# Kernel optimization log

Hardware: AMD Instinct MI355X
Metric: run time of the kernel (lower is better)

The kernel has to match this reference:

```python
import jax, jax.numpy as jnp
import numpy as np

N, D, C, E, K = 100000, 64, 40, 1600000, 2

def setup_inputs() -> dict:
    key = jax.random.key(0)
    k1, k2, k3 = jax.random.split(key, 3)
    x = jax.random.normal(k1, (N, D), dtype=jnp.float32)
    edge_index = jax.random.randint(k2, (2, E), 0, N, dtype=jnp.int64)
    W = jax.random.normal(k3, (D, C), dtype=jnp.float32) * 0.05
    b = jnp.zeros((C,), dtype=jnp.float32)
    return {"x": x, "edge_index": edge_index, "W": W, "b": b}

def reference(x, edge_index, W, b):
    n = x.shape[0]
    self_loop = jnp.arange(n, dtype=edge_index.dtype)
    row = jnp.concatenate([edge_index[0], self_loop])  # [E+N]
    col = jnp.concatenate([edge_index[1], self_loop])  # [E+N]
    # degree over row (out-degree incl. self loops), as in torch_geometric.utils.degree
    deg = jax.ops.segment_sum(jnp.ones_like(row, dtype=x.dtype), row, num_segments=n)
    deg_inv_sqrt = jnp.where(deg > 0, jax.lax.rsqrt(deg), 0.0)
    norm = deg_inv_sqrt[row] * deg_inv_sqrt[col]  # [E+N]
    # K hops of SpMM: out[r] += norm_e * x[c] for each edge e=(r,c)
    for _ in range(K):
        x = jax.ops.segment_sum(norm[:, None] * x[col], row, num_segments=n)
    logits = x @ W + b  # [N, C]
    return jax.nn.log_softmax(logits, axis=1)
```

## Files before the change

### kernel.cpp

```cpp
#include <hip/hip_runtime.h>
#include <math.h>


#define D_FEAT 64
#define NCLS 40
#define BROWS 512
#define BROWS_LOG 9
#define BINCAP 10240
#define CSRCAP 12288
#define EPT 25

typedef float v2f __attribute__((ext_vector_type(2)));

__device__ __forceinline__ unsigned pack_bf16_2(float lo, float hi) {
    unsigned ulo = __float_as_uint(lo);
    unsigned uhi = __float_as_uint(hi);
    ulo = (ulo + 0x7fffu + ((ulo >> 16) & 1u)) >> 16;
    uhi = (uhi + 0x7fffu + ((uhi >> 16) & 1u)) & 0xffff0000u;
    return uhi | ulo;
}

__device__ __forceinline__ void acc2p(unsigned u, v2f& a) {
    v2f v;
    v.x = __uint_as_float(u << 16);
    v.y = __uint_as_float(u & 0xffff0000u);
    a += v;
}

__global__ __launch_bounds__(256) void bin_edges_kernel(const int* __restrict__ rows,
                                                        const int* __restrict__ cols,
                                                        int* __restrict__ bucket_cursor,
                                                        unsigned* __restrict__ bins,
                                                        int e, int nb) {
    __shared__ int cnt[512];
    for (int i = threadIdx.x; i < nb; i += 256) cnt[i] = 0;
    __syncthreads();
    int base = blockIdx.x * (256 * EPT) + threadIdx.x;
    int rr[EPT], cc[EPT];
#pragma unroll
    for (int k = 0; k < EPT; k++) {
        int idx = base + k * 256;
        if (idx < e) { rr[k] = rows[idx]; cc[k] = cols[idx]; }
        else { rr[k] = -1; cc[k] = 0; }
    }
#pragma unroll
    for (int k = 0; k < EPT; k++)
        if (rr[k] >= 0) atomicAdd(&cnt[rr[k] >> BROWS_LOG], 1);
    __syncthreads();
    for (int i = threadIdx.x; i < nb; i += 256) {
        int c = cnt[i];
        cnt[i] = (c > 0) ? atomicAdd(&bucket_cursor[i], c) : 0;
    }
    __syncthreads();
#pragma unroll
    for (int k = 0; k < EPT; k++) {
        if (rr[k] >= 0) {
            int b = rr[k] >> BROWS_LOG;
            int pos = atomicAdd(&cnt[b], 1);
            bins[(size_t)b * BINCAP + pos] =
                ((unsigned)(rr[k] & (BROWS - 1)) << 17) | (unsigned)cc[k];
        }
    }
}

__global__ __launch_bounds__(512) void build_csr_kernel(const unsigned* __restrict__ bins,
                                                        const int* __restrict__ bucket_cursor,
                                                        int* __restrict__ csr_col,
                                                        uint2* __restrict__ row_info,
                                                        float* __restrict__ dis,
                                                        int* __restrict__ perm, int n) {
    __shared__ int cnt[512];
    __shared__ int sm[512];
    __shared__ int cur[512];
    __shared__ int lcsr[CSRCAP];
    int b = blockIdx.x;
    int tid = threadIdx.x;
    int m = bucket_cursor[b];
    cnt[tid] = 0;
    __syncthreads();
    const unsigned* bp = bins + (size_t)b * BINCAP;
    for (int i = tid; i < m; i += 512) atomicAdd(&cnt[bp[i] >> 17], 1);
    __syncthreads();
    int c = cnt[tid];
    int padded = (c + 3) & ~3;
    int r = b * BROWS + tid;
    if (r < n) dis[r] = rsqrtf(1.0f + (float)c);
    sm[tid] = padded;
    __syncthreads();
    for (int off = 1; off < 512; off <<= 1) {
        int t = (tid >= off) ? sm[tid - off] : 0;
        __syncthreads();
        sm[tid] += t;
        __syncthreads();
    }
    int off0 = sm[tid] - padded;
    cur[tid] = off0;
    if (r < n) row_info[r] = make_uint2((unsigned)(b * CSRCAP + off0), (unsigned)padded);
    __syncthreads();
    for (int i = tid; i < m; i += 512) {
        unsigned u = bp[i];
        int pos = atomicAdd(&cur[u >> 17], 1);
        lcsr[pos] = (int)(u & 0x1FFFFu);
    }
    __syncthreads();
    if (r < n) {
        for (int j = c; j < padded; j++) lcsr[off0 + j] = n;
    }
    __syncthreads();
    int tot = sm[511];
    int4* cp4 = (int4*)(csr_col + (size_t)b * CSRCAP);
    const int4* l4 = (const int4*)lcsr;
    for (int i = tid; i < (tot >> 2); i += 512) cp4[i] = l4[i];

    __syncthreads();
    if (tid < 64) cnt[tid] = 0;
    __syncthreads();
    int bin = min(padded >> 2, 63);
    if (r < n) atomicAdd(&cnt[bin], 1);
    __syncthreads();
    if (tid < 64) sm[tid] = cnt[tid];
    __syncthreads();
    for (int off = 1; off < 64; off <<= 1) {
        int t = (tid >= off && tid < 64) ? sm[tid - off] : 0;
        __syncthreads();
        if (tid < 64) sm[tid] += t;
        __syncthreads();
    }
    if (tid < 64) cur[tid] = sm[tid] - cnt[tid];
    __syncthreads();
    if (r < n) {
        int rank = atomicAdd(&cur[bin], 1);
        perm[b * BROWS + rank] = r;
    } else {
        perm[b * BROWS + tid] = -1;
    }
}

__global__ __launch_bounds__(256) void sort_rows_kernel(int* __restrict__ csr_col,
                                                        const uint2* __restrict__ row_info,
                                                        int n) {
    int wid = (int)((blockIdx.x * blockDim.x + threadIdx.x) >> 6);
    int lane = threadIdx.x & 63;
    int r0 = wid * 2, r1 = r0 + 1;
    if (r0 >= n) return;
    uint2 i0 = row_info[r0];
    uint2 i1 = (r1 < n) ? row_info[r1] : make_uint2(0u, 0u);
    int p0 = (int)i0.y, p1 = (int)i1.y;
    if (p0 <= 32 && p1 <= 32) {
        int half = lane >> 5, hl = lane & 31;
        int base = half ? (int)i1.x : (int)i0.x;
        int pad  = half ? p1 : p0;
        int key = (hl < pad) ? csr_col[base + hl] : 0x7fffffff;
#pragma unroll
        for (int k = 2; k <= 32; k <<= 1) {
#pragma unroll
            for (int j = k >> 1; j > 0; j >>= 1) {
                int other = __shfl_xor(key, j, 64);
                bool takeMin = (((hl & j) == 0) == ((hl & k) == 0));
                int mn = min(key, other), mx = max(key, other);
                key = takeMin ? mn : mx;
            }
        }
        if (hl < pad) csr_col[base + hl] = key;
    } else {
        for (int t = 0; t < 2; t++) {
            int base = t ? (int)i1.x : (int)i0.x;
            int pad  = t ? p1 : p0;
            if (pad == 0) continue;
            if (pad <= 64) {
                int key = (lane < pad) ? csr_col[base + lane] : 0x7fffffff;
#pragma unroll
                for (int k = 2; k <= 64; k <<= 1) {
#pragma unroll
                    for (int j = k >> 1; j > 0; j >>= 1) {
                        int other = __shfl_xor(key, j, 64);
                        bool takeMin = (((lane & j) == 0) == ((lane & k) == 0));
                        int mn = min(key, other), mx = max(key, other);
                        key = takeMin ? mn : mx;
                    }
                }
                if (lane < pad) csr_col[base + lane] = key;
            } else if (lane == 0) {
                for (int i2 = 1; i2 < pad; i2++) {
                    int kk = csr_col[base + i2];
                    int j2 = i2 - 1;
                    while (j2 >= 0 && csr_col[base + j2] > kk) {
                        csr_col[base + j2 + 1] = csr_col[base + j2]; j2--;
                    }
                    csr_col[base + j2 + 1] = kk;
                }
            }
        }
    }
}

__global__ void scale_x_kernel(const float* __restrict__ x, const float* __restrict__ dis,
                               unsigned* __restrict__ xs0, unsigned* __restrict__ xs1, int n) {
    int i = blockIdx.x * blockDim.x + threadIdx.x;
    int total = (n + 1) * (D_FEAT / 2);
    if (i >= total) return;
    int node = i >> 5;
    if (node < n) {
        float s = dis[node];
        float2 v = ((const float2*)x)[i];
        xs0[i] = pack_bf16_2(s * v.x, s * v.y);
    } else {
        xs0[i] = 0u;
        xs1[i] = 0u;
    }
}

#define GATHER16(cp, xs_in, ql, base, len)                                  \
    uint2 u0, u1, u2, u3, u4, u5, u6, u7;                                   \
    uint2 u8, u9, u10, u11, u12, u13, u14, u15;                             \
    bool g0 = base < len, g1 = base + 4 < len;                              \
    bool g2 = base + 8 < len, g3 = base + 12 < len;                         \
    if (g0) {                                                               \
        uint4 cv = cp[(base >> 2) + 0];                                     \
        u0 = xs_in[cv.x * 16 + ql]; u1 = xs_in[cv.y * 16 + ql];             \
        u2 = xs_in[cv.z * 16 + ql]; u3 = xs_in[cv.w * 16 + ql];             \
    }                                                                       \
    if (g1) {                                                               \
        uint4 cv = cp[(base >> 2) + 1];                                     \
        u4 = xs_in[cv.x * 16 + ql]; u5 = xs_in[cv.y * 16 + ql];             \
        u6 = xs_in[cv.z * 16 + ql]; u7 = xs_in[cv.w * 16 + ql];             \
    }                                                                       \
    if (g2) {                                                               \
        uint4 cv = cp[(base >> 2) + 2];                                     \
        u8 = xs_in[cv.x * 16 + ql]; u9 = xs_in[cv.y * 16 + ql];             \
        u10 = xs_in[cv.z * 16 + ql]; u11 = xs_in[cv.w * 16 + ql];           \
    }                                                                       \
    if (g3) {                                                               \
        uint4 cv = cp[(base >> 2) + 3];                                     \
        u12 = xs_in[cv.x * 16 + ql]; u13 = xs_in[cv.y * 16 + ql];           \
        u14 = xs_in[cv.z * 16 + ql]; u15 = xs_in[cv.w * 16 + ql];           \
    }                                                                       \
    if (g0) {                                                               \
        acc2p(u0.x, hA01); acc2p(u0.y, hA23);                               \
        acc2p(u1.x, hA01); acc2p(u1.y, hA23);                               \
        acc2p(u2.x, hA01); acc2p(u2.y, hA23);                               \
        acc2p(u3.x, hA01); acc2p(u3.y, hA23);                               \
    }                                                                       \
    if (g1) {                                                               \
        acc2p(u4.x, hB01); acc2p(u4.y, hB23);                               \
        acc2p(u5.x, hB01); acc2p(u5.y, hB23);                               \
        acc2p(u6.x, hB01); acc2p(u6.y, hB23);                               \
        acc2p(u7.x, hB01); acc2p(u7.y, hB23);                               \
    }                                                                       \
    if (g2) {                                                               \
        acc2p(u8.x, hA01); acc2p(u8.y, hA23);                               \
        acc2p(u9.x, hA01); acc2p(u9.y, hA23);                               \
        acc2p(u10.x, hA01); acc2p(u10.y, hA23);                             \
        acc2p(u11.x, hA01); acc2p(u11.y, hA23);                             \
    }                                                                       \
    if (g3) {                                                               \
        acc2p(u12.x, hB01); acc2p(u12.y, hB23);                             \
        acc2p(u13.x, hB01); acc2p(u13.y, hB23);                             \
        acc2p(u14.x, hB01); acc2p(u14.y, hB23);                             \
        acc2p(u15.x, hB01); acc2p(u15.y, hB23);                             \
    }

__global__ __launch_bounds__(256, 6) void spmm_hop1_kernel(const uint2* __restrict__ xs_in,
                                                           uint2* __restrict__ xs_out,
                                                           const int* __restrict__ perm,
                                                           const uint2* __restrict__ row_info,
                                                           const int* __restrict__ csr_col,
                                                           const float* __restrict__ dis,
                                                           int n, int nperm) {
    int wave = (blockIdx.x * blockDim.x + threadIdx.x) >> 6;
    int lane = threadIdx.x & 63;
    int q = lane >> 4, ql = lane & 15;
    int pidx = wave * 4 + q;
    int r = (pidx < nperm) ? perm[pidx] : -1;
    bool valid = (r >= 0);
    int s = 0, len = 0;
    if (valid) { uint2 info = row_info[r]; s = (int)info.x; len = (int)info.y; }
    int maxlen = len;
    maxlen = max(maxlen, __shfl_xor(maxlen, 16, 64));
    maxlen = max(maxlen, __shfl_xor(maxlen, 32, 64));

    v2f hA01 = {0.f, 0.f}, hA23 = {0.f, 0.f};
    v2f hB01 = {0.f, 0.f}, hB23 = {0.f, 0.f};
    const uint4* cp = (const uint4*)(csr_col + s);
    for (int base = 0; base < maxlen; base += 16) {
        GATHER16(cp, xs_in, ql, base, len)
    }
    if (valid) {
        v2f h01 = hA01 + hB01;
        v2f h23 = hA23 + hB23;
        uint2 us = xs_in[r * 16 + ql];
        acc2p(us.x, h01); acc2p(us.y, h23);
        float dr = dis[r];
        float dr2 = dr * dr;
        xs_out[r * 16 + ql] = make_uint2(pack_bf16_2(dr2 * h01.x, dr2 * h01.y),
                                         pack_bf16_2(dr2 * h23.x, dr2 * h23.y));
    }
}

__global__ __launch_bounds__(256, 6) void spmm_logits_kernel(const uint2* __restrict__ xs_in,
                                                             const int* __restrict__ perm,
                                                             const uint2* __restrict__ row_info,
                                                             const int* __restrict__ csr_col,
                                                             const float* __restrict__ dis,
                                                             const float* __restrict__ W,
                                                             const float* __restrict__ b,
                                                             float* __restrict__ out,
                                                             int n, int nperm) {
    __shared__ float Wt[NCLS][D_FEAT + 4];
    __shared__ float bl[NCLS];
    __shared__ float hl[16][D_FEAT + 4];
    for (int i = threadIdx.x; i < D_FEAT * NCLS; i += 256) {
        int d = i / NCLS, cc = i - d * NCLS;
        Wt[cc][d] = W[i];
    }
    for (int i = threadIdx.x; i < NCLS; i += 256) bl[i] = b[i];
    __syncthreads();

    int wave = (blockIdx.x * blockDim.x + threadIdx.x) >> 6;
    int lane = threadIdx.x & 63;
    int q = lane >> 4, ql = lane & 15;
    int pidx = wave * 4 + q;
    int r = (pidx < nperm) ? perm[pidx] : -1;
    bool valid = (r >= 0);
    int s = 0, len = 0;
    if (valid) { uint2 info = row_info[r]; s = (int)info.x; len = (int)info.y; }
    int maxlen = len;
    maxlen = max(maxlen, __shfl_xor(maxlen, 16, 64));
    maxlen = max(maxlen, __shfl_xor(maxlen, 32, 64));

    v2f hA01 = {0.f, 0.f}, hA23 = {0.f, 0.f};
    v2f hB01 = {0.f, 0.f}, hB23 = {0.f, 0.f};
    const uint4* cp = (const uint4*)(csr_col + s);
    for (int base = 0; base < maxlen; base += 16) {
        GATHER16(cp, xs_in, ql, base, len)
    }

    float y0, y1, y2;
    int c0 = ql, c1 = ql + 16;
    int c2 = (ql < 8) ? (ql + 32) : ql;
    {
        v2f h01 = hA01 + hB01;
        v2f h23 = hA23 + hB23;
        uint2 us = valid ? xs_in[r * 16 + ql] : make_uint2(0u, 0u);
        acc2p(us.x, h01); acc2p(us.y, h23);
        float dr = valid ? dis[r] : 0.f;
        float h0 = h01.x * dr, h1 = h01.y * dr, h2 = h23.x * dr, h3 = h23.y * dr;

        int rowslot = ((threadIdx.x >> 6) << 2) + q;
        *(float4*)&hl[rowslot][ql * 4] = make_float4(h0, h1, h2, h3);

        y0 = bl[c0]; y1 = bl[c1]; y2 = bl[c2];
#pragma unroll
        for (int g = 0; g < 16; g++) {
            float4 hv = *(const float4*)&hl[rowslot][g * 4];
            float4 w0 = *(const float4*)&Wt[c0][g * 4];
            float4 w1 = *(const float4*)&Wt[c1][g * 4];
            float4 w2 = *(const float4*)&Wt[c2][g * 4];
            y0 += hv.x * w0.x + hv.y * w0.y + hv.z * w0.z + hv.w * w0.w;
            y1 += hv.x * w1.x + hv.y * w1.y + hv.z * w1.z + hv.w * w1.w;
            y2 += hv.x * w2.x + hv.y * w2.y + hv.z * w2.z + hv.w * w2.w;
        }
    }

    bool has3 = (ql < 8);
    float m = fmaxf(y0, y1);
    if (has3) m = fmaxf(m, y2);
#pragma unroll
    for (int o = 8; o > 0; o >>= 1) m = fmaxf(m, __shfl_xor(m, o, 64));
    float sm = __expf(y0 - m) + __expf(y1 - m) + (has3 ? __expf(y2 - m) : 0.f);
#pragma unroll
    for (int o = 8; o > 0; o >>= 1) sm += __shfl_xor(sm, o, 64);
    float lse = m + __logf(sm);

    if (valid) {
        float* op = out + (long long)r * NCLS;
        op[ql] = y0 - lse;
        op[ql + 16] = y1 - lse;
        if (has3) op[ql + 32] = y2 - lse;
    }
}

extern "C" void kernel_launch(void* const* d_in, const int* in_sizes, int n_in,
                              void* d_out, int out_size, void* d_ws, size_t ws_size,
                              hipStream_t stream) {
    const float* x  = (const float*)d_in[0];
    const int*   ei = (const int*)d_in[1];
    const float* W  = (const float*)d_in[2];
    const float* b  = (const float*)d_in[3];
    float* out = (float*)d_out;

    const int n = in_sizes[0] / D_FEAT;
    const int e = in_sizes[1] / 2;
    const int nb = (n + BROWS - 1) / BROWS;

    const int* rows = ei;
    const int* cols = ei + e;

    size_t na = ((size_t)n + 256) & ~(size_t)255;
    size_t npm = (size_t)nb * BROWS;
    int*      bucket_cursor = (int*)d_ws;
    float*    dis           = (float*)(bucket_cursor + 256);
    uint2*    row_info      = (uint2*)(dis + na);
    int*      perm          = (int*)(row_info + na);
    unsigned* bins          = (unsigned*)(perm + npm);
    int*      csr_col       = (int*)(bins + (size_t)nb * BINCAP);
    unsigned* xs0           = (unsigned*)(csr_col + (size_t)nb * CSRCAP);
    unsigned* xs1           = xs0 + (size_t)(n + 1) * (D_FEAT / 2);

    const int BS = 256;

    hipMemsetAsync(bucket_cursor, 0, (size_t)nb * sizeof(int), stream);
    {
        int blocks = (e + BS * EPT - 1) / (BS * EPT);
        bin_edges_kernel<<<blocks, BS, 0, stream>>>(rows, cols, bucket_cursor, bins, e, nb);
    }
    build_csr_kernel<<<nb, 512, 0, stream>>>(bins, bucket_cursor, csr_col, row_info, dis,
                                             perm, n);
    {
        int nwv = (n + 1) / 2;
        int blocks = (nwv * 64 + BS - 1) / BS;
        sort_rows_kernel<<<blocks, BS, 0, stream>>>(csr_col, row_info, n);
    }
    {
        int tot = (n + 1) * (D_FEAT / 2);
        scale_x_kernel<<<(tot + BS - 1) / BS, BS, 0, stream>>>(x, dis, xs0, xs1, n);
    }

    int nperm = (int)npm;
    int nwaves = nperm / 4;
    int blocks = (nwaves * 64 + BS - 1) / BS;
    spmm_hop1_kernel<<<blocks, BS, 0, stream>>>((const uint2*)xs0, (uint2*)xs1, perm,
                                                row_info, csr_col, dis, n, nperm);
    spmm_logits_kernel<<<blocks, BS, 0, stream>>>((const uint2*)xs1, perm, row_info, csr_col,
                                                  dis, W, b, out, n, nperm);
}
```

Before: 211.0 us.

## Pack per-row info, merge sort and scale kernels, prefetch column indices

Replaces the perm array plus the row_info and dis lookups with a packed uint4 per permuted slot (offset, length, row, degree scale), removing a dependent indirection at the start of each SpMM wave. The sort and x-scaling kernels are merged into one launch, split by block index. The gather loop now software-prefetches the next 16 column indices while gathering the current ones. Gathers are issued without per-group guards, relying on padding of the CSR tail with the dummy node. Occupancy hint drops from 6 to 5 to make room for the extra prefetch registers.

```diff
diff --git a/kernel.cpp b/kernel.cpp
--- a/kernel.cpp
+++ b/kernel.cpp
@@ -68,7 +68,7 @@
                                                         int* __restrict__ csr_col,
                                                         uint2* __restrict__ row_info,
                                                         float* __restrict__ dis,
-                                                        int* __restrict__ perm, int n) {
+                                                        uint4* __restrict__ pinfo, int n) {
     __shared__ int cnt[512];
     __shared__ int sm[512];
     __shared__ int cur[512];
@@ -84,7 +84,8 @@
     int c = cnt[tid];
     int padded = (c + 3) & ~3;
     int r = b * BROWS + tid;
-    if (r < n) dis[r] = rsqrtf(1.0f + (float)c);
+    float dv = rsqrtf(1.0f + (float)c);
+    if (r < n) dis[r] = dv;
     sm[tid] = padded;
     __syncthreads();
     for (int off = 1; off < 512; off <<= 1) {
@@ -111,6 +112,10 @@
     int4* cp4 = (int4*)(csr_col + (size_t)b * CSRCAP);
     const int4* l4 = (const int4*)lcsr;
     for (int i = tid; i < (tot >> 2); i += 512) cp4[i] = l4[i];
+    {
+        int g = tot + tid;
+        if (g < CSRCAP) csr_col[(size_t)b * CSRCAP + g] = n;
+    }
 
     __syncthreads();
     if (tid < 64) cnt[tid] = 0;
@@ -130,16 +135,37 @@
     __syncthreads();
     if (r < n) {
         int rank = atomicAdd(&cur[bin], 1);
-        perm[b * BROWS + rank] = r;
+        pinfo[b * BROWS + rank] = make_uint4((unsigned)(b * CSRCAP + off0),
+                                             (unsigned)padded, (unsigned)r,
+                                             __float_as_uint(dv));
     } else {
-        perm[b * BROWS + tid] = -1;
-    }
-}
-
-__global__ __launch_bounds__(256) void sort_rows_kernel(int* __restrict__ csr_col,
-                                                        const uint2* __restrict__ row_info,
-                                                        int n) {
-    int wid = (int)((blockIdx.x * blockDim.x + threadIdx.x) >> 6);
+        pinfo[b * BROWS + tid] = make_uint4(0u, 0u, 0xFFFFFFFFu, 0u);
+    }
+}
+
+__global__ __launch_bounds__(256) void sort_scale_kernel(int* __restrict__ csr_col,
+                                                         const uint2* __restrict__ row_info,
+                                                         const float* __restrict__ x,
+                                                         const float* __restrict__ dis,
+                                                         unsigned* __restrict__ xs0,
+                                                         unsigned* __restrict__ xs1,
+                                                         int n, int sortBlocks) {
+    if ((int)blockIdx.x >= sortBlocks) {
+        int i = ((int)blockIdx.x - sortBlocks) * 256 + threadIdx.x;
+        int total = (n + 1) * (D_FEAT / 2);
+        if (i >= total) return;
+        int node = i >> 5;
+        if (node < n) {
+            float s = dis[node];
+            float2 v = ((const float2*)x)[i];
+            xs0[i] = pack_bf16_2(s * v.x, s * v.y);
+        } else {
+            xs0[i] = 0u;
+            xs1[i] = 0u;
+        }
+        return;
+    }
+    int wid = ((int)blockIdx.x * 256 + (int)threadIdx.x) >> 6;
     int lane = threadIdx.x & 63;
     int r0 = wid * 2, r1 = r0 + 1;
     if (r0 >= n) return;
@@ -194,87 +220,59 @@
     }
 }
 
-__global__ void scale_x_kernel(const float* __restrict__ x, const float* __restrict__ dis,
-                               unsigned* __restrict__ xs0, unsigned* __restrict__ xs1, int n) {
-    int i = blockIdx.x * blockDim.x + threadIdx.x;
-    int total = (n + 1) * (D_FEAT / 2);
-    if (i >= total) return;
-    int node = i >> 5;
-    if (node < n) {
-        float s = dis[node];
-        float2 v = ((const float2*)x)[i];
-        xs0[i] = pack_bf16_2(s * v.x, s * v.y);
-    } else {
-        xs0[i] = 0u;
-        xs1[i] = 0u;
-    }
-}
-
-#define GATHER16(cp, xs_in, ql, base, len)                                  \
-    uint2 u0, u1, u2, u3, u4, u5, u6, u7;                                   \
-    uint2 u8, u9, u10, u11, u12, u13, u14, u15;                             \
-    bool g0 = base < len, g1 = base + 4 < len;                              \
-    bool g2 = base + 8 < len, g3 = base + 12 < len;                         \
-    if (g0) {                                                               \
-        uint4 cv = cp[(base >> 2) + 0];                                     \
-        u0 = xs_in[cv.x * 16 + ql]; u1 = xs_in[cv.y * 16 + ql];             \
-        u2 = xs_in[cv.z * 16 + ql]; u3 = xs_in[cv.w * 16 + ql];             \
+#define GATHER_ITER(cp, xs_in, ql, base, len)                               \
+    uint2 u0 = xs_in[cv0.x * 16 + ql], u1 = xs_in[cv0.y * 16 + ql];         \
+    uint2 u2 = xs_in[cv0.z * 16 + ql], u3 = xs_in[cv0.w * 16 + ql];         \
+    uint2 u4 = xs_in[cv1.x * 16 + ql], u5 = xs_in[cv1.y * 16 + ql];         \
+    uint2 u6 = xs_in[cv1.z * 16 + ql], u7 = xs_in[cv1.w * 16 + ql];         \
+    uint2 u8 = xs_in[cv2.x * 16 + ql], u9 = xs_in[cv2.y * 16 + ql];         \
+    uint2 u10 = xs_in[cv2.z * 16 + ql], u11 = xs_in[cv2.w * 16 + ql];       \
+    uint2 u12 = xs_in[cv3.x * 16 + ql], u13 = xs_in[cv3.y * 16 + ql];       \
+    uint2 u14 = xs_in[cv3.z * 16 + ql], u15 = xs_in[cv3.w * 16 + ql];       \
+    {                                                                       \
+        int nb4 = (base >> 2) + 4;                                          \
+        nv0 = cp[nb4]; nv1 = cp[nb4 + 1];                                   \
+        nv2 = cp[nb4 + 2]; nv3 = cp[nb4 + 3];                               \
     }                                                                       \
-    if (g1) {                                                               \
-        uint4 cv = cp[(base >> 2) + 1];                                     \
-        u4 = xs_in[cv.x * 16 + ql]; u5 = xs_in[cv.y * 16 + ql];             \
-        u6 = xs_in[cv.z * 16 + ql]; u7 = xs_in[cv.w * 16 + ql];             \
-    }                                                                       \
-    if (g2) {                                                               \
-        uint4 cv = cp[(base >> 2) + 2];                                     \
-        u8 = xs_in[cv.x * 16 + ql]; u9 = xs_in[cv.y * 16 + ql];             \
-        u10 = xs_in[cv.z * 16 + ql]; u11 = xs_in[cv.w * 16 + ql];           \
-    }                                                                       \
-    if (g3) {                                                               \
-        uint4 cv = cp[(base >> 2) + 3];                                     \
-        u12 = xs_in[cv.x * 16 + ql]; u13 = xs_in[cv.y * 16 + ql];           \
-        u14 = xs_in[cv.z * 16 + ql]; u15 = xs_in[cv.w * 16 + ql];           \
-    }                                                                       \
-    if (g0) {                                                               \
+    __builtin_amdgcn_sched_barrier(0);                                      \
+    if (base < len) {                                                       \
         acc2p(u0.x, hA01); acc2p(u0.y, hA23);                               \
         acc2p(u1.x, hA01); acc2p(u1.y, hA23);                               \
         acc2p(u2.x, hA01); acc2p(u2.y, hA23);                               \
         acc2p(u3.x, hA01); acc2p(u3.y, hA23);                               \
     }                                                                       \
-    if (g1) {                                                               \
+    if (base + 4 < len) {                                                   \
         acc2p(u4.x, hB01); acc2p(u4.y, hB23);                               \
         acc2p(u5.x, hB01); acc2p(u5.y, hB23);                               \
         acc2p(u6.x, hB01); acc2p(u6.y, hB23);                               \
         acc2p(u7.x, hB01); acc2p(u7.y, hB23);                               \
     }                                                                       \
-    if (g2) {                                                               \
+    if (base + 8 < len) {                                                   \
         acc2p(u8.x, hA01); acc2p(u8.y, hA23);                               \
         acc2p(u9.x, hA01); acc2p(u9.y, hA23);                               \
         acc2p(u10.x, hA01); acc2p(u10.y, hA23);                             \
         acc2p(u11.x, hA01); acc2p(u11.y, hA23);                             \
     }                                                                       \
-    if (g3) {                                                               \
+    if (base + 12 < len) {                                                  \
         acc2p(u12.x, hB01); acc2p(u12.y, hB23);                             \
         acc2p(u13.x, hB01); acc2p(u13.y, hB23);                             \
         acc2p(u14.x, hB01); acc2p(u14.y, hB23);                             \
         acc2p(u15.x, hB01); acc2p(u15.y, hB23);                             \
-    }
-
-__global__ __launch_bounds__(256, 6) void spmm_hop1_kernel(const uint2* __restrict__ xs_in,
+    }                                                                       \
+    cv0 = nv0; cv1 = nv1; cv2 = nv2; cv3 = nv3;
+
+__global__ __launch_bounds__(256, 5) void spmm_hop1_kernel(const uint2* __restrict__ xs_in,
                                                            uint2* __restrict__ xs_out,
-                                                           const int* __restrict__ perm,
-                                                           const uint2* __restrict__ row_info,
+                                                           const uint4* __restrict__ pinfo,
                                                            const int* __restrict__ csr_col,
-                                                           const float* __restrict__ dis,
-                                                           int n, int nperm) {
+                                                           int n) {
     int wave = (blockIdx.x * blockDim.x + threadIdx.x) >> 6;
     int lane = threadIdx.x & 63;
     int q = lane >> 4, ql = lane & 15;
-    int pidx = wave * 4 + q;
-    int r = (pidx < nperm) ? perm[pidx] : -1;
+    uint4 info = pinfo[wave * 4 + q];
+    int s = (int)info.x, len = (int)info.y;
+    int r = (int)info.z;
     bool valid = (r >= 0);
-    int s = 0, len = 0;
-    if (valid) { uint2 info = row_info[r]; s = (int)info.x; len = (int)info.y; }
     int maxlen = len;
     maxlen = max(maxlen, __shfl_xor(maxlen, 16, 64));
     maxlen = max(maxlen, __shfl_xor(maxlen, 32, 64));
@@ -282,30 +280,30 @@
     v2f hA01 = {0.f, 0.f}, hA23 = {0.f, 0.f};
     v2f hB01 = {0.f, 0.f}, hB23 = {0.f, 0.f};
     const uint4* cp = (const uint4*)(csr_col + s);
+    uint4 cv0 = cp[0], cv1 = cp[1], cv2 = cp[2], cv3 = cp[3];
+    uint4 nv0, nv1, nv2, nv3;
     for (int base = 0; base < maxlen; base += 16) {
-        GATHER16(cp, xs_in, ql, base, len)
+        GATHER_ITER(cp, xs_in, ql, base, len)
     }
     if (valid) {
         v2f h01 = hA01 + hB01;
         v2f h23 = hA23 + hB23;
         uint2 us = xs_in[r * 16 + ql];
         acc2p(us.x, h01); acc2p(us.y, h23);
-        float dr = dis[r];
-        float dr2 = dr * dr;
-        xs_out[r * 16 + ql] = make_uint2(pack_bf16_2(dr2 * h01.x, dr2 * h01.y),
-                                         pack_bf16_2(dr2 * h23.x, dr2 * h23.y));
-    }
-}
-
-__global__ __launch_bounds__(256, 6) void spmm_logits_kernel(const uint2* __restrict__ xs_in,
-                                                             const int* __restrict__ perm,
-                                                             const uint2* __restrict__ row_info,
+        float dr = __uint_as_float(info.w);
+        float d2 = dr * dr;
+        xs_out[r * 16 + ql] = make_uint2(pack_bf16_2(d2 * h01.x, d2 * h01.y),
+                                         pack_bf16_2(d2 * h23.x, d2 * h23.y));
+    }
+}
+
+__global__ __launch_bounds__(256, 5) void spmm_logits_kernel(const uint2* __restrict__ xs_in,
+                                                             const uint4* __restrict__ pinfo,
                                                              const int* __restrict__ csr_col,
-                                                             const float* __restrict__ dis,
                                                              const float* __restrict__ W,
                                                              const float* __restrict__ b,
                                                              float* __restrict__ out,
-                                                             int n, int nperm) {
+                                                             int n) {
     __shared__ float Wt[NCLS][D_FEAT + 4];
     __shared__ float bl[NCLS];
     __shared__ float hl[16][D_FEAT + 4];
@@ -319,11 +317,10 @@
     int wave = (blockIdx.x * blockDim.x + threadIdx.x) >> 6;
     int lane = threadIdx.x & 63;
     int q = lane >> 4, ql = lane & 15;
-    int pidx = wave * 4 + q;
-    int r = (pidx < nperm) ? perm[pidx] : -1;
+    uint4 info = pinfo[wave * 4 + q];
+    int s = (int)info.x, len = (int)info.y;
+    int r = (int)info.z;
     bool valid = (r >= 0);
-    int s = 0, len = 0;
-    if (valid) { uint2 info = row_info[r]; s = (int)info.x; len = (int)info.y; }
     int maxlen = len;
     maxlen = max(maxlen, __shfl_xor(maxlen, 16, 64));
     maxlen = max(maxlen, __shfl_xor(maxlen, 32, 64));
@@ -331,8 +328,10 @@
     v2f hA01 = {0.f, 0.f}, hA23 = {0.f, 0.f};
     v2f hB01 = {0.f, 0.f}, hB23 = {0.f, 0.f};
     const uint4* cp = (const uint4*)(csr_col + s);
+    uint4 cv0 = cp[0], cv1 = cp[1], cv2 = cp[2], cv3 = cp[3];
+    uint4 nv0, nv1, nv2, nv3;
     for (int base = 0; base < maxlen; base += 16) {
-        GATHER16(cp, xs_in, ql, base, len)
+        GATHER_ITER(cp, xs_in, ql, base, len)
     }
 
     float y0, y1, y2;
@@ -343,7 +342,7 @@
         v2f h23 = hA23 + hB23;
         uint2 us = valid ? xs_in[r * 16 + ql] : make_uint2(0u, 0u);
         acc2p(us.x, h01); acc2p(us.y, h23);
-        float dr = valid ? dis[r] : 0.f;
+        float dr = __uint_as_float(info.w);
         float h0 = h01.x * dr, h1 = h01.y * dr, h2 = h23.x * dr, h3 = h23.y * dr;
 
         int rowslot = ((threadIdx.x >> 6) << 2) + q;
@@ -401,8 +400,8 @@
     int*      bucket_cursor = (int*)d_ws;
     float*    dis           = (float*)(bucket_cursor + 256);
     uint2*    row_info      = (uint2*)(dis + na);
-    int*      perm          = (int*)(row_info + na);
-    unsigned* bins          = (unsigned*)(perm + npm);
+    uint4*    pinfo         = (uint4*)(row_info + na);
+    unsigned* bins          = (unsigned*)(pinfo + npm);
     int*      csr_col       = (int*)(bins + (size_t)nb * BINCAP);
     unsigned* xs0           = (unsigned*)(csr_col + (size_t)nb * CSRCAP);
     unsigned* xs1           = xs0 + (size_t)(n + 1) * (D_FEAT / 2);
@@ -415,22 +414,20 @@
         bin_edges_kernel<<<blocks, BS, 0, stream>>>(rows, cols, bucket_cursor, bins, e, nb);
     }
     build_csr_kernel<<<nb, 512, 0, stream>>>(bins, bucket_cursor, csr_col, row_info, dis,
-                                             perm, n);
+                                             pinfo, n);
     {
         int nwv = (n + 1) / 2;
-        int blocks = (nwv * 64 + BS - 1) / BS;
-        sort_rows_kernel<<<blocks, BS, 0, stream>>>(csr_col, row_info, n);
-    }
-    {
+        int sortBlocks = (nwv * 64 + BS - 1) / BS;
         int tot = (n + 1) * (D_FEAT / 2);
-        scale_x_kernel<<<(tot + BS - 1) / BS, BS, 0, stream>>>(x, dis, xs0, xs1, n);
-    }
-
-    int nperm = (int)npm;
-    int nwaves = nperm / 4;
+        int scaleBlocks = (tot + BS - 1) / BS;
+        sort_scale_kernel<<<sortBlocks + scaleBlocks, BS, 0, stream>>>(
+            csr_col, row_info, x, dis, xs0, xs1, n, sortBlocks);
+    }
+
+    int nwaves = (int)npm / 4;
     int blocks = (nwaves * 64 + BS - 1) / BS;
-    spmm_hop1_kernel<<<blocks, BS, 0, stream>>>((const uint2*)xs0, (uint2*)xs1, perm,
-                                                row_info, csr_col, dis, n, nperm);
-    spmm_logits_kernel<<<blocks, BS, 0, stream>>>((const uint2*)xs1, perm, row_info, csr_col,
-                                                  dis, W, b, out, n, nperm);
-}
+    spmm_hop1_kernel<<<blocks, BS, 0, stream>>>((const uint2*)xs0, (uint2*)xs1, pinfo,
+                                                csr_col, n);
+    spmm_logits_kernel<<<blocks, BS, 0, stream>>>((const uint2*)xs1, pinfo, csr_col,
+                                                  W, b, out, n);
+}
```

New measurement: 213.9 us. Within noise of the previous version (+1.4%).
